# Kernel tuning notes

Measured on AMD Instinct MI355X. Metric: run time of the kernel, lower is better.

Reference implementation:

```python
import jax, jax.numpy as jnp
import numpy as np

IN_CH = 4
OUT_CH = 64
T = 100            # max points per pillar
P_MAX = 12000      # max pillars
DX = 0.16
DY = 0.16
XMIN, YMIN, ZMIN, XMAX, YMAX, ZMAX = -40.0, -40.0, -3.0, 40.0, 40.0, 1.0
NX = int(round((XMAX - XMIN) / DX))   # 500
NY = int(round((YMAX - YMIN) / DY))   # 500
EPS = 1e-5
B, N = 2, 120000


def setup_inputs() -> dict:
    key = jax.random.key(0)
    ks = jax.random.split(key, 8)
    # realistic LiDAR-like cloud: x,y spread over the grid, z mostly in range
    xy = jax.random.normal(ks[0], (B, N, 2)) * 15.0
    z = jax.random.uniform(ks[1], (B, N, 1), minval=-3.2, maxval=1.2)
    inten = jax.random.uniform(ks[2], (B, N, 1))
    points = jnp.concatenate([xy, z, inten], axis=-1)

    def bn_params(k):
        k1, k2, k3, k4 = jax.random.split(k, 4)
        g = 1.0 + 0.1 * jax.random.normal(k1, (OUT_CH,))
        b = 0.1 * jax.random.normal(k2, (OUT_CH,))
        m = 0.1 * jax.random.normal(k3, (OUT_CH,))
        v = 0.5 + jax.random.uniform(k4, (OUT_CH,))
        return g, b, m, v

    w1 = jax.random.normal(ks[3], (OUT_CH, IN_CH + 4)) * 0.3
    w2 = jax.random.normal(ks[4], (OUT_CH, OUT_CH)) * 0.1
    g1, b1, m1, v1 = bn_params(ks[5])
    g2, b2, m2, v2 = bn_params(ks[6])
    return dict(points=points, w1=w1, g1=g1, b1=b1, m1=m1, v1=v1,
                w2=w2, g2=g2, b2=b2, m2=m2, v2=v2)


def _pillarize(pts):
    # pts: [N, 4] -> dense pillar tensor [P_MAX, T, 8], validity mask, pillar keys
    x, y, z = pts[:, 0], pts[:, 1], pts[:, 2]
    valid = (x >= XMIN) & (x < XMAX) & (y >= YMIN) & (y < YMAX) & (z >= ZMIN) & (z < ZMAX)
    xi = jnp.clip(jnp.floor((x - XMIN) / DX), 0, NX - 1).astype(jnp.int32)
    yi = jnp.clip(jnp.floor((y - YMIN) / DY), 0, NY - 1).astype(jnp.int32)
    big = jnp.int32(NX * NY)  # sentinel key for invalid points (sorts last)
    keyv = jnp.where(valid, xi * NY + yi, big)
    order = jnp.argsort(keyv)          # stable sort == torch.unique ordering
    sk = keyv[order]
    ps = pts[order]
    vs = sk < big
    n = pts.shape[0]
    idx = jnp.arange(n, dtype=jnp.int32)
    new = vs & jnp.concatenate([jnp.ones((1,), bool), sk[1:] != sk[:-1]])
    rank = jnp.cumsum(new.astype(jnp.int32)) - 1          # dense pillar id (sorted)
    p_eff = jnp.minimum(jnp.sum(new.astype(jnp.int32)), P_MAX)
    start = jax.lax.cummax(jnp.where(new, idx, jnp.int32(-1)))
    intra = idx - start                                   # slot within pillar
    keep = vs & (rank < P_MAX) & (intra < T)
    r = jnp.where(keep, rank, P_MAX)
    t = jnp.where(keep, intra, T)
    pillar_pts = jnp.zeros((P_MAX, T, IN_CH), pts.dtype).at[r, t].set(ps, mode='drop')
    keys = jnp.zeros((P_MAX,), jnp.int32).at[r].set(sk, mode='drop')
    pvalid = jnp.arange(P_MAX, dtype=jnp.int32) < p_eff
    xi_u = (keys // NY).astype(pts.dtype)
    yi_u = (keys % NY).astype(pts.dtype)
    xc = xi_u * DX + XMIN + DX / 2
    yc = yi_u * DY + YMIN + DY / 2
    # enhanced features are computed for ALL T slots (incl. empty), like the original
    x_off = pillar_pts[:, :, 0] - xc[:, None]
    y_off = pillar_pts[:, :, 1] - yc[:, None]
    xc_t = jnp.broadcast_to(xc[:, None], (P_MAX, T))
    yc_t = jnp.broadcast_to(yc[:, None], (P_MAX, T))
    enh = jnp.stack([xc_t, yc_t, x_off, y_off], axis=-1)
    pin = jnp.concatenate([pillar_pts, enh], axis=-1)     # [P_MAX, T, 8]
    return pin, pvalid, keys


def _forward(points, w1, g1, b1, m1, v1, w2, g2, b2, m2, v2):
    pin, pvalid, keys = jax.vmap(_pillarize)(points)      # [B, P_MAX, T, 8]

    def bn(h, g, b, m, v):
        return (h - m) * (g * jax.lax.rsqrt(v + EPS)) + b

    h = jax.nn.relu(bn(jnp.einsum('bptc,oc->bpto', pin, w1), g1, b1, m1, v1))
    h = jax.nn.relu(bn(jnp.einsum('bptc,oc->bpto', h, w2), g2, b2, m2, v2))
    feats = jnp.max(h, axis=2)                            # max-pool over T
    feats = jnp.where(pvalid[..., None], feats, 0.0)      # zero-pad unused pillars
    bidx = jnp.broadcast_to(jnp.arange(points.shape[0], dtype=jnp.int32)[:, None], pvalid.shape)
    xi_u = jnp.where(pvalid, keys // NY, 0)
    yi_u = jnp.where(pvalid, keys % NY, 0)
    coords = jnp.stack([bidx, xi_u, yi_u], axis=-1)       # [B, P_MAX, 3]
    return feats, coords


def reference(points, w1, g1, b1, m1, v1, w2, g2, b2, m2, v2):
    return _forward(points, w1, g1, b1, m1, v1, w2, g2, b2, m2, v2)
```

## Files before the change

### kernel.cpp

```cpp
#include <hip/hip_runtime.h>
#include <stdint.h>
#include <stddef.h>

#define NBATCH 2
#define NPTS   120000
#define T_SLOTS 100
#define PMAX   12000
#define NXG    500
#define NYG    500
#define NBINS  (NXG*NYG)
#define NCH    ((NBINS + 63)/64)
#define NG     ((NCH + 63)/64)

#define FEAT_BLOCKS 3000

#define WS_FLAGS   ((size_t)0)
#define WS_SLOT    (WS_FLAGS + (size_t)NBATCH*NBINS)
#define WS_ZEROEND (WS_SLOT  + (size_t)NBATCH*PMAX*4)
#define WS_MASKS   (WS_ZEROEND)
#define WS_PDAT    (WS_MASKS + (size_t)NBATCH*NCH*8)
#define WS_CHOFF   (WS_PDAT  + (size_t)NBATCH*PMAX*T_SLOTS*16)
#define WS_PILKEY  (WS_CHOFF + (size_t)NBATCH*NCH*4)
#define WS_GRPS    (WS_PILKEY+ (size_t)NBATCH*PMAX*4)
#define WS_PTOT    (WS_GRPS  + (size_t)NBATCH*NG*4)
#define WS_NEEDED  (WS_PTOT  + (size_t)NBATCH*4)

#define ZERO_F4    (WS_ZEROEND / 16)


__global__ void k_zero(float4* __restrict__ dst) {
    int i = blockIdx.x * blockDim.x + threadIdx.x;
    if (i < (int)ZERO_F4) {
        float4 z; z.x = 0.0f; z.y = 0.0f; z.z = 0.0f; z.w = 0.0f;
        dst[i] = z;
    }
}

__global__ void k_key(const float4* __restrict__ pts4,
                      unsigned char* __restrict__ flags) {
    int i = blockIdx.x * blockDim.x + threadIdx.x;
    if (i >= NBATCH * NPTS) return;
    int b = i / NPTS;
    float4 P = pts4[i];
    float x = P.x, y = P.y, z = P.z;
    bool valid = (x >= -40.0f) && (x < 40.0f) &&
                 (y >= -40.0f) && (y < 40.0f) &&
                 (z >= -3.0f)  && (z < 1.0f);
    if (valid) {
        float fx = floorf((x + 40.0f) / 0.16f);
        float fy = floorf((y + 40.0f) / 0.16f);
        fx = fminf(fmaxf(fx, 0.0f), (float)(NXG - 1));
        fy = fminf(fmaxf(fy, 0.0f), (float)(NYG - 1));
        int key = (int)fx * NYG + (int)fy;
        flags[(size_t)b * NBINS + key] = 1;
    }
}

__global__ __launch_bounds__(1024)
void k_scanA(const unsigned char* __restrict__ flags,
             unsigned long long* __restrict__ masks,
             int* __restrict__ grpsum) {
    __shared__ int scnt[64];
    const int g    = blockIdx.x;
    const int b    = blockIdx.y;
    const int tid  = threadIdx.x;
    const int lane = tid & 63;
    const int w    = tid >> 6;
    const unsigned char* fb = flags + (size_t)b * NBINS;

    #pragma unroll
    for (int q = 0; q < 4; ++q) {
        int chl = w * 4 + q;
        int ch  = g * 64 + chl;
        int bin = ch * 64 + lane;
        int pres = (ch < NCH && bin < NBINS && fb[bin]) ? 1 : 0;
        unsigned long long m = __ballot(pres);
        if (lane == 0) {
            if (ch < NCH) masks[(size_t)b * NCH + ch] = m;
            scnt[chl] = __popcll(m);
        }
    }
    __syncthreads();
    if (w == 0) {
        int v = scnt[lane];
        #pragma unroll
        for (int off = 32; off > 0; off >>= 1) v += __shfl_xor(v, off);
        if (lane == 0) grpsum[b * NG + g] = v;
    }
}

__global__ void k_choff(const unsigned long long* __restrict__ masks,
                        const int* __restrict__ grpsum,
                        int* __restrict__ choff, int* __restrict__ ptot) {
    int tid  = threadIdx.x;
    int lane = tid & 63;
    int gw   = blockIdx.x * 4 + (tid >> 6);
    if (gw >= NBATCH * NG) return;
    int b = gw / NG, g = gw - b * NG;

    int gs = (lane < NG) ? grpsum[b * NG + lane] : 0;
    int incl = gs;
    #pragma unroll
    for (int off = 1; off < 64; off <<= 1) {
        int t2 = __shfl_up(incl, off);
        if (lane >= off) incl += t2;
    }
    int tot  = __shfl(incl, NG - 1);
    int goff = __shfl(incl, (g == 0) ? 0 : g - 1);
    if (g == 0) goff = 0;
    if (g == 0 && lane == 0) ptot[b] = tot;

    int ch = g * 64 + lane;
    int cs = (ch < NCH) ? __popcll(masks[(size_t)b * NCH + ch]) : 0;
    int incl2 = cs;
    #pragma unroll
    for (int off = 1; off < 64; off <<= 1) {
        int t2 = __shfl_up(incl2, off);
        if (lane >= off) incl2 += t2;
    }
    if (ch < NCH) choff[(size_t)b * NCH + ch] = goff + incl2 - cs;
}

__global__ void k_fill(const float4* __restrict__ pts4,
                       const unsigned long long* __restrict__ masks,
                       const int* __restrict__ choff, int* __restrict__ slotctr,
                       int* __restrict__ pilkey, float4* __restrict__ pdat) {
    int i = blockIdx.x * blockDim.x + threadIdx.x;
    if (i >= NBATCH * NPTS) return;
    int b = i / NPTS;
    float4 P = pts4[i];
    float x = P.x, y = P.y, z = P.z;
    bool valid = (x >= -40.0f) && (x < 40.0f) &&
                 (y >= -40.0f) && (y < 40.0f) &&
                 (z >= -3.0f)  && (z < 1.0f);
    if (!valid) return;
    float fx = floorf((x + 40.0f) / 0.16f);
    float fy = floorf((y + 40.0f) / 0.16f);
    fx = fminf(fmaxf(fx, 0.0f), (float)(NXG - 1));
    fy = fminf(fmaxf(fy, 0.0f), (float)(NYG - 1));
    int key = (int)fx * NYG + (int)fy;

    int ch = key >> 6;
    unsigned long long m = masks[(size_t)b * NCH + ch];
    int r = choff[(size_t)b * NCH + ch] +
            __popcll(m & ((1ULL << (key & 63)) - 1ULL));
    if (r >= PMAX) return;
    pilkey[b * PMAX + r] = key;
    int t = atomicAdd(&slotctr[b * PMAX + r], 1);
    if (t < T_SLOTS)
        pdat[((size_t)(b * PMAX + r)) * T_SLOTS + t] = P;
}

__global__ __launch_bounds__(256, 8)
void k_feats(const float4* __restrict__ pdat,
             const float* __restrict__ w1, const float* __restrict__ g1,
             const float* __restrict__ b1, const float* __restrict__ m1,
             const float* __restrict__ v1,
             const float* __restrict__ w2, const float* __restrict__ g2,
             const float* __restrict__ b2, const float* __restrict__ m2,
             const float* __restrict__ v2,
             const int* __restrict__ pilkey, const int* __restrict__ slotctr,
             const int* __restrict__ ptot, float* __restrict__ out) {
    __shared__ float4 w2s[16 * 64];
    __shared__ __align__(16) float h1s[4][2][64];

    const int tid  = threadIdx.x;
    const int lane = tid & 63;
    const int widx = tid >> 6;
    const int o = lane;

    float* feats  = out;
    float* coords = out + (size_t)NBATCH * PMAX * 64;

    const int r  = blockIdx.x * 4 + widx;
    const int pA = r;
    const int pB = r + PMAX;

    const float4* prowA = pdat + (size_t)pA * T_SLOTS;
    const float4* prowB = pdat + (size_t)pB * T_SLOTS;
    int keyA = pilkey[pA], keyB = pilkey[pB];
    int cA   = slotctr[pA], cB = slotctr[pB];
    int pe0 = ptot[0]; if (pe0 > PMAX) pe0 = PMAX;
    int pe1 = ptot[1]; if (pe1 > PMAX) pe1 = PMAX;

    float s1 = g1[o] * rsqrtf(v1[o] + 1e-5f);
    float b1f = b1[o] - m1[o] * s1;
    float w1r[8];
    {
        const float4* w14 = (const float4*)(w1 + o * 8);
        float4 a = w14[0], c4 = w14[1];
        w1r[0] = a.x * s1;  w1r[1] = a.y * s1;  w1r[2] = a.z * s1;  w1r[3] = a.w * s1;
        w1r[4] = c4.x * s1; w1r[5] = c4.y * s1; w1r[6] = c4.z * s1; w1r[7] = c4.w * s1;
    }
    float wx = w1r[0] + w1r[6];
    float wy = w1r[1] + w1r[7];

    float s2 = g2[o] * rsqrtf(v2[o] + 1e-5f);
    float b2f = b2[o] - m2[o] * s2;
    {
        const float4* w2row = (const float4*)(w2 + o * 64);
        #pragma unroll
        for (int it = 0; it < 4; ++it) {
            int kq = widx + it * 4;
            float4 t = w2row[kq];
            t.x *= s2; t.y *= s2; t.z *= s2; t.w *= s2;
            w2s[kq * 64 + o] = t;
        }
    }
    __syncthreads();

    int xiA = keyA / NYG, yiA = keyA - xiA * NYG;
    int xiB = keyB / NYG, yiB = keyB - xiB * NYG;
    float xcA = (float)xiA * 0.16f - 40.0f + 0.08f;
    float ycA = (float)yiA * 0.16f - 40.0f + 0.08f;
    float xcB = (float)xiB * 0.16f - 40.0f + 0.08f;
    float ycB = (float)yiB * 0.16f - 40.0f + 0.08f;
    float pbA = b1f + (w1r[4] - w1r[6]) * xcA + (w1r[5] - w1r[7]) * ycA;
    float pbB = b1f + (w1r[4] - w1r[6]) * xcB + (w1r[5] - w1r[7]) * ycB;

    bool liveA = (r < pe0), liveB = (r < pe1);
    int pcA = liveA ? ((cA < T_SLOTS) ? cA : T_SLOTS) : 0;
    int pcB = liveB ? ((cB < T_SLOTS) ? cB : T_SLOTS) : 0;
    int nItA = liveA ? (pcA + ((cA < T_SLOTS) ? 1 : 0)) : 0;
    int nItB = liveB ? (pcB + ((cB < T_SLOTS) ? 1 : 0)) : 0;
    int maxN = (nItA > nItB) ? nItA : nItB;

    float accA = 0.0f, accB = 0.0f;

    for (int s = 0; s < maxN; ++s) {
        float4 PA, PB;
        if (s < pcA) PA = prowA[s];
        else { PA.x = 0.0f; PA.y = 0.0f; PA.z = 0.0f; PA.w = 0.0f; }
        if (s < pcB) PB = prowB[s];
        else { PB.x = 0.0f; PB.y = 0.0f; PB.z = 0.0f; PB.w = 0.0f; }

        float hA = pbA;
        hA += wx * PA.x; hA += wy * PA.y;
        hA += w1r[2] * PA.z; hA += w1r[3] * PA.w;
        hA = fmaxf(hA, 0.0f);
        float hB = pbB;
        hB += wx * PB.x; hB += wy * PB.y;
        hB += w1r[2] * PB.z; hB += w1r[3] * PB.w;
        hB = fmaxf(hB, 0.0f);

        h1s[widx][0][o] = hA;
        h1s[widx][1][o] = hB;
        asm volatile("s_waitcnt lgkmcnt(0)" ::: "memory");

        float aA0 = b2f, aA1 = 0.0f, aB0 = b2f, aB1 = 0.0f;
        #pragma unroll
        for (int kq = 0; kq < 16; ++kq) {
            float4 w  = w2s[kq * 64 + o];
            float4 qA = *(const float4*)&h1s[widx][0][kq * 4];
            float4 qB = *(const float4*)&h1s[widx][1][kq * 4];
            aA0 += w.x * qA.x; aA1 += w.y * qA.y;
            aA0 += w.z * qA.z; aA1 += w.w * qA.w;
            aB0 += w.x * qB.x; aB1 += w.y * qB.y;
            aB0 += w.z * qB.z; aB1 += w.w * qB.w;
        }
        if (s < nItA) accA = fmaxf(accA, fmaxf(aA0 + aA1, 0.0f));
        if (s < nItB) accB = fmaxf(accB, fmaxf(aB0 + aB1, 0.0f));
    }

    size_t frowA = (size_t)pA * 64, crowA = (size_t)pA * 3;
    size_t frowB = (size_t)pB * 64, crowB = (size_t)pB * 3;
    feats[frowA + o] = liveA ? accA : 0.0f;
    feats[frowB + o] = liveB ? accB : 0.0f;
    if (o < 3) {
        coords[crowA + o] = liveA
            ? ((o == 0) ? 0.0f : (o == 1) ? (float)xiA : (float)yiA)
            : 0.0f;
        coords[crowB + o] = liveB
            ? ((o == 0) ? 1.0f : (o == 1) ? (float)xiB : (float)yiB)
            : ((o == 0) ? 1.0f : 0.0f);
    }
}


extern "C" void kernel_launch(void* const* d_in, const int* in_sizes, int n_in,
                              void* d_out, int out_size, void* d_ws, size_t ws_size,
                              hipStream_t stream) {
    if (ws_size < WS_NEEDED) return;

    const float4* pts4 = (const float4*)d_in[0];
    const float* w1  = (const float*)d_in[1];
    const float* g1  = (const float*)d_in[2];
    const float* b1  = (const float*)d_in[3];
    const float* m1  = (const float*)d_in[4];
    const float* v1  = (const float*)d_in[5];
    const float* w2  = (const float*)d_in[6];
    const float* g2  = (const float*)d_in[7];
    const float* b2  = (const float*)d_in[8];
    const float* m2  = (const float*)d_in[9];
    const float* v2  = (const float*)d_in[10];

    char* ws = (char*)d_ws;
    unsigned char* flags = (unsigned char*)(ws + WS_FLAGS);
    int*  slotctr = (int*)(ws + WS_SLOT);
    unsigned long long* masks = (unsigned long long*)(ws + WS_MASKS);
    float4* pdat  = (float4*)(ws + WS_PDAT);
    int*  choff   = (int*)(ws + WS_CHOFF);
    int*  pilkey  = (int*)(ws + WS_PILKEY);
    int*  grpsum  = (int*)(ws + WS_GRPS);
    int*  ptot    = (int*)(ws + WS_PTOT);
    float* out    = (float*)d_out;

    dim3 blk256(256);
    int npt = NBATCH * NPTS;
    dim3 grdPts((npt + 255) / 256);

    hipLaunchKernelGGL(k_zero, dim3((ZERO_F4 + 255) / 256), blk256, 0, stream,
                       (float4*)(ws + WS_FLAGS));

    hipLaunchKernelGGL(k_key, grdPts, blk256, 0, stream, pts4, flags);

    hipLaunchKernelGGL(k_scanA, dim3(NG, NBATCH), dim3(1024), 0, stream,
                       flags, masks, grpsum);

    hipLaunchKernelGGL(k_choff, dim3((NBATCH * NG + 3) / 4), blk256, 0, stream,
                       masks, grpsum, choff, ptot);

    hipLaunchKernelGGL(k_fill, grdPts, blk256, 0, stream,
                       pts4, masks, choff, slotctr, pilkey, pdat);

    hipLaunchKernelGGL(k_feats, dim3(FEAT_BLOCKS), blk256, 0, stream,
                       pdat, w1, g1, b1, m1, v1, w2, g2, b2, m2, v2,
                       pilkey, slotctr, ptot, out);
}
```

Before: 43.17 us.

## Fuse chunk-offset scan into scan kernel via last-block ticket

Merges the separate chunk-offset kernel into the flag-scan kernel. A global atomic ticket picks the last finishing block, which then computes the group and chunk prefix sums for both batches. Zeroing of the slot counters moves from the zero kernel into the scan kernel, so the zero pass clears less memory. This removes one kernel launch and its inter-kernel gap, at the cost of threadfences, an atomic, and a serial tail done by a single block.

```diff
diff --git a/kernel.cpp b/kernel.cpp
--- a/kernel.cpp
+++ b/kernel.cpp
@@ -15,9 +15,10 @@
 #define FEAT_BLOCKS 3000
 
 #define WS_FLAGS   ((size_t)0)
-#define WS_SLOT    (WS_FLAGS + (size_t)NBATCH*NBINS)
-#define WS_ZEROEND (WS_SLOT  + (size_t)NBATCH*PMAX*4)
-#define WS_MASKS   (WS_ZEROEND)
+#define WS_TICKET  (WS_FLAGS + (size_t)NBATCH*NBINS)
+#define WS_ZEROEND (WS_TICKET + 16)
+#define WS_SLOT    (WS_ZEROEND)
+#define WS_MASKS   (WS_SLOT  + (size_t)NBATCH*PMAX*4)
 #define WS_PDAT    (WS_MASKS + (size_t)NBATCH*NCH*8)
 #define WS_CHOFF   (WS_PDAT  + (size_t)NBATCH*PMAX*T_SLOTS*16)
 #define WS_PILKEY  (WS_CHOFF + (size_t)NBATCH*NCH*4)
@@ -57,16 +58,25 @@
 }
 
 __global__ __launch_bounds__(1024)
-void k_scanA(const unsigned char* __restrict__ flags,
-             unsigned long long* __restrict__ masks,
-             int* __restrict__ grpsum) {
+void k_scan(const unsigned char* __restrict__ flags,
+            unsigned long long* __restrict__ masks,
+            int* __restrict__ grpsum, int* __restrict__ choff,
+            int* __restrict__ ptot, int* __restrict__ ticket,
+            int* __restrict__ slotctr) {
     __shared__ int scnt[64];
+    __shared__ int goff_s[NBATCH][64];
+    __shared__ int amLast;
     const int g    = blockIdx.x;
     const int b    = blockIdx.y;
     const int tid  = threadIdx.x;
     const int lane = tid & 63;
     const int w    = tid >> 6;
     const unsigned char* fb = flags + (size_t)b * NBINS;
+
+    {
+        int idx = (b * NG + g) * 1024 + tid;
+        if (idx < NBATCH * PMAX) slotctr[idx] = 0;
+    }
 
     #pragma unroll
     for (int q = 0; q < 4; ++q) {
@@ -87,38 +97,46 @@
         for (int off = 32; off > 0; off >>= 1) v += __shfl_xor(v, off);
         if (lane == 0) grpsum[b * NG + g] = v;
     }
-}
-
-__global__ void k_choff(const unsigned long long* __restrict__ masks,
-                        const int* __restrict__ grpsum,
-                        int* __restrict__ choff, int* __restrict__ ptot) {
-    int tid  = threadIdx.x;
-    int lane = tid & 63;
-    int gw   = blockIdx.x * 4 + (tid >> 6);
-    if (gw >= NBATCH * NG) return;
-    int b = gw / NG, g = gw - b * NG;
-
-    int gs = (lane < NG) ? grpsum[b * NG + lane] : 0;
-    int incl = gs;
-    #pragma unroll
-    for (int off = 1; off < 64; off <<= 1) {
-        int t2 = __shfl_up(incl, off);
-        if (lane >= off) incl += t2;
-    }
-    int tot  = __shfl(incl, NG - 1);
-    int goff = __shfl(incl, (g == 0) ? 0 : g - 1);
-    if (g == 0) goff = 0;
-    if (g == 0 && lane == 0) ptot[b] = tot;
-
-    int ch = g * 64 + lane;
-    int cs = (ch < NCH) ? __popcll(masks[(size_t)b * NCH + ch]) : 0;
-    int incl2 = cs;
-    #pragma unroll
-    for (int off = 1; off < 64; off <<= 1) {
-        int t2 = __shfl_up(incl2, off);
-        if (lane >= off) incl2 += t2;
-    }
-    if (ch < NCH) choff[(size_t)b * NCH + ch] = goff + incl2 - cs;
+    __syncthreads();
+
+    if (tid == 0) {
+        __threadfence();
+        int t = atomicAdd(ticket, 1);
+        amLast = (t == NBATCH * NG - 1);
+    }
+    __syncthreads();
+    if (!amLast) return;
+    __threadfence();
+
+    if (w < NBATCH) {
+        int bb = w;
+        int v = (lane < NG) ? grpsum[bb * NG + lane] : 0;
+        int incl = v;
+        #pragma unroll
+        for (int off = 1; off < 64; off <<= 1) {
+            int t2 = __shfl_up(incl, off);
+            if (lane >= off) incl += t2;
+        }
+        if (lane < NG) goff_s[bb][lane] = incl - v;
+        if (lane == NG - 1) ptot[bb] = incl;
+    }
+    __syncthreads();
+
+    for (int bb = 0; bb < NBATCH; ++bb) {
+        for (int gg = w; gg < NG; gg += 16) {
+            int ch = gg * 64 + lane;
+            unsigned long long m = (ch < NCH) ? masks[(size_t)bb * NCH + ch] : 0ULL;
+            int cs = __popcll(m);
+            int ex = cs;
+            #pragma unroll
+            for (int off = 1; off < 64; off <<= 1) {
+                int t2 = __shfl_up(ex, off);
+                if (lane >= off) ex += t2;
+            }
+            ex -= cs;
+            if (ch < NCH) choff[(size_t)bb * NCH + ch] = goff_s[bb][gg] + ex;
+        }
+    }
 }
 
 __global__ void k_fill(const float4* __restrict__ pts4,
@@ -296,6 +314,7 @@
 
     char* ws = (char*)d_ws;
     unsigned char* flags = (unsigned char*)(ws + WS_FLAGS);
+    int*  ticket  = (int*)(ws + WS_TICKET);
     int*  slotctr = (int*)(ws + WS_SLOT);
     unsigned long long* masks = (unsigned long long*)(ws + WS_MASKS);
     float4* pdat  = (float4*)(ws + WS_PDAT);
@@ -314,11 +333,8 @@
 
     hipLaunchKernelGGL(k_key, grdPts, blk256, 0, stream, pts4, flags);
 
-    hipLaunchKernelGGL(k_scanA, dim3(NG, NBATCH), dim3(1024), 0, stream,
-                       flags, masks, grpsum);
-
-    hipLaunchKernelGGL(k_choff, dim3((NBATCH * NG + 3) / 4), blk256, 0, stream,
-                       masks, grpsum, choff, ptot);
+    hipLaunchKernelGGL(k_scan, dim3(NG, NBATCH), dim3(1024), 0, stream,
+                       flags, masks, grpsum, choff, ptot, ticket, slotctr);
 
     hipLaunchKernelGGL(k_fill, grdPts, blk256, 0, stream,
                        pts4, masks, choff, slotctr, pilkey, pdat);
```

Result: slower. 51.58 us (+19.5%).
